# Kernel tuning notes

Hardware: AMD Instinct MI355X
Metric: run time of the kernel (lower is better)

Reference implementation:

```python
import jax, jax.numpy as jnp
import numpy as np

IMG = 14          # image_x_y_dim
STRIDE = 4        # stride == kernel_size == n_qubits
H_MAT = jnp.array([[1.0, 1.0], [1.0, -1.0]], dtype=jnp.complex64) / np.sqrt(2.0)
_RZ_SIGNS = jnp.array([-0.5j, 0.5j], dtype=jnp.complex64)


def _apply_1q(state, U, w):
    # contract 2x2 gate U into wire-axis w of state with shape (2,)*n
    s = jnp.tensordot(U, state, axes=[[1], [w]])
    return jnp.moveaxis(s, 0, w)


def _rz(state, theta, w, n):
    d = jnp.exp(_RZ_SIGNS * theta)  # diag(e^{-i t/2}, e^{i t/2})
    shape = [1] * n
    shape[w] = 2
    return state * d.reshape(shape)


def _rx(state, theta, w):
    c = jnp.cos(0.5 * theta).astype(jnp.complex64)
    s = ((-1j) * jnp.sin(0.5 * theta)).astype(jnp.complex64)
    U = jnp.stack([jnp.stack([c, s]), jnp.stack([s, c])])
    return _apply_1q(state, U, w)


def _ry(state, theta, w):
    c = jnp.cos(0.5 * theta).astype(jnp.complex64)
    s = jnp.sin(0.5 * theta).astype(jnp.complex64)
    U = jnp.stack([jnp.stack([c, -s]), jnp.stack([s, c])])
    return _apply_1q(state, U, w)


def _crz(state, theta, cw, tw, n):
    # PennyLane CRZ: diag(1, 1, e^{-i t/2}, e^{i t/2}) in |control, target> basis
    d = jnp.exp(_RZ_SIGNS * theta)
    P = jnp.stack([jnp.ones(2, jnp.complex64), d])  # axes: (control, target)
    if cw > tw:
        P = P.T
    a, b = min(cw, tw), max(cw, tw)
    shape = [1] * n
    shape[a] = 2
    shape[b] = 2
    return state * P.reshape(shape)


def _zexp(state, n):
    probs = state.real ** 2 + state.imag ** 2
    outs = []
    for w in range(n):
        shape = [1] * n
        shape[w] = 2
        sgn = jnp.array([1.0, -1.0], jnp.float32).reshape(shape)
        outs.append(jnp.sum(probs * sgn))
    return jnp.stack(outs)  # (n,)


def _circuit4(x, weights):
    # x: (L,) with L in {4, 8, 16}; weights: (2, 8)
    n, vpq, L = 4, 4, x.shape[0]
    state = jnp.zeros((2,) * n, jnp.complex64).at[(0,) * n].set(1.0)
    for q in range(n):  # encoding: H then alternating RZ/RX per qubit
        state = _apply_1q(state, H_MAT, q)
        for i in range(vpq):
            idx = q * vpq + i
            if idx < L:
                state = _rz(state, x[idx], q, n) if i % 2 == 0 else _rx(state, x[idx], q)
    for l in range(2):  # n_layers
        for i in range(n):
            state = _crz(state, weights[l, i], i, (i + 1) % n, n)
        for j in range(n, 2 * n):
            state = _ry(state, weights[l, j], j % n)
    return _zexp(state, n)  # (4,)


def _circuit8(x, weights):
    # x: (64,); weights: (3, 16); angles scaled by pi as in qnn_circuit
    n, L = 8, 64
    vpq = L // n + 1  # 9
    state = jnp.zeros((2,) * n, jnp.complex64).at[(0,) * n].set(1.0)
    for q in range(n):
        state = _apply_1q(state, H_MAT, q)
        for i in range(vpq):
            idx = q * vpq + i
            if idx < L:
                theta = np.pi * x[idx]
                state = _rz(state, theta, q, n) if i % 2 == 0 else _rx(state, theta, q)
    for l in range(3):  # qnn_layers
        for i in range(n):
            state = _crz(state, weights[l, i], i, (i + 1) % n, n)
        for j in range(n, 2 * n):
            state = _ry(state, weights[l, j], j % n)
    return _zexp(state, n)  # (8,)


def _forward_single(x196, w1, w2, fc_w, fc_b):
    img = x196.reshape(IMG, IMG)
    feats = []
    for i in range(0, IMG, STRIDE):
        for j in range(0, IMG, STRIDE):
            patch = img[i:i + 4, j:j + 4].reshape(-1)  # edge patches truncate to 8 or 4
            feats.append(_circuit4(patch, w1))
    f = jnp.concatenate(feats)       # (64,)
    g = _circuit8(f, w2)             # (8,)
    return fc_w @ g + fc_b           # (3,)


def setup_inputs() -> dict:
    key = jax.random.key(0)
    k0, k1, k2, k3, k4 = jax.random.split(key, 5)
    bs = 8192
    X = jax.random.normal(k0, (bs, 196), jnp.float32)
    w1 = jax.random.uniform(k1, (2, 8), jnp.float32, 0.0, 2.0 * np.pi)
    w2 = jax.random.uniform(k2, (3, 16), jnp.float32, 0.0, 2.0 * np.pi)
    fc_w = jax.random.normal(k3, (3, 8), jnp.float32) / np.sqrt(8.0)
    fc_b = jax.random.normal(k4, (3,), jnp.float32) * 0.01
    return {"X": X, "w1": w1, "w2": w2, "fc_w": fc_w, "fc_b": fc_b}


def reference(X, w1, w2, fc_w, fc_b):
    return jax.vmap(_forward_single, in_axes=(0, None, None, None, None))(X, w1, w2, fc_w, fc_b)
```

## Files before the change

kernel.cpp:

```cpp
#include <hip/hip_runtime.h>

#define DEV __device__ __forceinline__

namespace {

typedef float f32x2 __attribute__((ext_vector_type(2)));

DEV f32x2 splat(float x){ f32x2 r; r.x = x; r.y = x; return r; }
DEV f32x2 csw(f32x2 a){ return __builtin_shufflevector(a, a, 1, 0); }
DEV f32x2 cmulv(f32x2 a, f32x2 b){
  f32x2 nt; nt.x = -b.y; nt.y = b.x;
  return splat(a.x)*b + splat(a.y)*nt;
}
DEV f32x2 cphase(f32x2 a, f32x2 cv, f32x2 sv){ return cv*a + sv*csw(a); }
DEV void halfsc(float th, float& c, float& s){ __sincosf(0.5f*th, &s, &c); }

constexpr float RSQRT2 = 0.70710678118654752440f;
constexpr float PI_F   = 3.14159265358979323846f;

template<int CTRL> DEV float qperm(float v){
  return __int_as_float(__builtin_amdgcn_mov_dpp(__float_as_int(v), CTRL, 0xF, 0xF, true));
}
template<int OFF> DEV float swzf(float v){
  return __int_as_float(__builtin_amdgcn_ds_swizzle(__float_as_int(v), OFF));
}
template<int B> DEV float shfx(float v){
  if constexpr (B==1)      return qperm<0xB1>(v);
  else if constexpr (B==2) return qperm<0x4E>(v);
  else if constexpr (B==4) return swzf<0x101F>(v);
  else if constexpr (B==8) return qperm<0x128>(v);
  else                     return swzf<0x401F>(v);
}

template<int NA> DEV void build_psi(f32x2 (&v)[2], const float* ang, float scale){
  v[0].x = RSQRT2; v[0].y = 0.f;
  v[1].x = RSQRT2; v[1].y = 0.f;
  #pragma unroll
  for (int i = 0; i < NA; ++i){
    float c, s; halfsc(scale * ang[i], c, s);
    f32x2 cv = splat(c);
    f32x2 sp; sp.x = s;  sp.y = -s;
    if ((i & 1) == 0){
      f32x2 sn; sn.x = -s; sn.y = s;
      v[0] = cv*v[0] + sp*csw(v[0]);
      v[1] = cv*v[1] + sn*csw(v[1]);
    } else {
      f32x2 t0 = csw(v[0]), t1 = csw(v[1]);
      v[0] = cv*v[0] + sp*t1;
      v[1] = cv*v[1] + sp*t0;
    }
  }
}

template<int S> DEV void ry_loc8(f32x2 (&a)[8], float2 cs){
  const float c = cs.x, s = cs.y;
  #pragma unroll
  for (int m = 0; m < 8; ++m) if (!(m & S)) {
    f32x2 u = a[m], v = a[m|S];
    a[m]   = splat(c)*u - splat(s)*v;
    a[m|S] = splat(s)*u + splat(c)*v;
  }
}
template<int MASK> DEV void ry_lane8(f32x2 (&a)[8], int r, float2 cs){
  const float c = cs.x;
  const float sg = (r & MASK) ? cs.y : -cs.y;
  #pragma unroll
  for (int m = 0; m < 8; ++m){
    f32x2 o; o.x = shfx<MASK>(a[m].x); o.y = shfx<MASK>(a[m].y);
    a[m] = splat(c)*a[m] + splat(sg)*o;
  }
}

DEV f32x2 tov(float2 v){ f32x2 r; r.x = v.x; r.y = v.y; return r; }

}

__global__ __launch_bounds__(256, 4)
void qnn_fused_kernel(const float* __restrict__ X,  const float* __restrict__ w1,
                      const float* __restrict__ w2, const float* __restrict__ fcw,
                      const float* __restrict__ fcb, float* __restrict__ out, int bs)
{
  __shared__ float4 Xlds4[8*49];
  __shared__ float  feats[8][80];
  __shared__ float4 p1chain[8][16][5];
  __shared__ float4 chain2[8][9];
  __shared__ float4 p1phi[2][2][8];
  __shared__ float2 p1ry[2][4];
  __shared__ float2 ryw[3][8];
  __shared__ float4 phi2[3*32*9];

  const int t  = threadIdx.x;
  const int sl = t >> 5;
  const int r  = t & 31;
  int sample = blockIdx.x * 8 + sl;
  if (sample >= bs) sample = bs - 1;

  {
    const float4* X4 = (const float4*)X;
    for (int idx = t; idx < 8*49; idx += 256){
      int s_ = idx / 49, e = idx - s_*49;
      int gs = blockIdx.x * 8 + s_;
      if (gs >= bs) gs = bs - 1;
      Xlds4[idx] = X4[(size_t)gs*49 + e];
    }
  }
  if (t < 32){
    const int l = t >> 4, Lb = (t >> 3) & 1, m = t & 7;
    const float h0 = 0.5f*w1[l*8+0], h1 = 0.5f*w1[l*8+1];
    const float h2 = 0.5f*w1[l*8+2], h3 = 0.5f*w1[l*8+3];
    const bool m4 = m & 4, m2 = m & 2, m1 = m & 1;
    float phi = 0.f;
    phi += Lb ? (m4 ? h0 : -h0) : 0.f;
    phi += m4 ? (m2 ? h1 : -h1) : 0.f;
    phi += m2 ? (m1 ? h2 : -h2) : 0.f;
    phi += m1 ? (Lb ? h3 : -h3) : 0.f;
    float c, s; __sincosf(phi, &s, &c);
    p1phi[l][Lb][m] = {c, c, -s, s};
  } else if (t < 40){
    const int j = t - 32, l = j >> 2, i = j & 3;
    float c, s; halfsc(w1[l*8 + 4 + i], c, s); p1ry[l][i] = {c, s};
  } else if (t < 64){
    const int j = t - 40, l = j >> 3, i = j & 7;
    float c, s; halfsc(w2[l*16 + 8 + i], c, s); ryw[l][i] = {c, s};
  }
  for (int idx = t; idx < 3*256; idx += 256){
    const int l = idx >> 8, rr = (idx >> 3) & 31, mm = idx & 7;
    const float* wl = w2 + l*16;
    const float h0 = 0.5f*wl[0], h1 = 0.5f*wl[1], h2 = 0.5f*wl[2], h3 = 0.5f*wl[3];
    const float h4 = 0.5f*wl[4], h5 = 0.5f*wl[5], h6 = 0.5f*wl[6], h7 = 0.5f*wl[7];
    const bool b16 = rr & 16, b8 = rr & 8, b4 = rr & 4, b2 = rr & 2, b1 = rr & 1;
    const bool m4 = mm & 4, m2 = mm & 2, m1 = mm & 1;
    float phi = 0.f;
    phi += b16 ? (b8 ? h0 : -h0) : 0.f;
    phi += b8  ? (b4 ? h1 : -h1) : 0.f;
    phi += b4  ? (b2 ? h2 : -h2) : 0.f;
    phi += b2  ? (b1 ? h3 : -h3) : 0.f;
    phi += b1  ? (m4 ? h4 : -h4) : 0.f;
    phi += m4  ? (m2 ? h5 : -h5) : 0.f;
    phi += m2  ? (m1 ? h6 : -h6) : 0.f;
    phi += m1  ? (b16 ? h7 : -h7) : 0.f;
    float c, s; __sincosf(phi, &s, &c);
    phi2[(l*32 + rr)*9 + mm] = {c, c, -s, s};
  }
  __syncthreads();

  #pragma unroll
  for (int jj = 0; jj < 2; ++jj){
    const int j = t + jj*256;
    const int s_ = j >> 6, p = (j >> 2) & 15, q = j & 3;
    const int pi = p >> 2, pj = p & 3;
    const int shift = (pj == 3) ? 1 : 2;
    const int cmask = (1 << shift) - 1;
    const int limit = ((pi == 3) ? 2 : 4) << shift;
    const float* Xf = (const float*)Xlds4 + s_*196;
    float ang[4];
    #pragma unroll
    for (int i = 0; i < 4; ++i){
      const int k = q*4 + i;
      int idx = (pi*4 + (k >> shift))*14 + pj*4 + (k & cmask);
      idx = idx > 195 ? 195 : idx;
      float v = Xf[idx];
      ang[i] = (k < limit) ? v : 0.f;
    }
    f32x2 v[2];
    build_psi<4>(v, ang, 1.0f);
    p1chain[s_][p][q] = {v[0].x, v[0].y, v[1].x, v[1].y};
  }
  __syncthreads();

  {
    const int p = r >> 1, Lb = r & 1;
    f32x2 ps[4][2];
    #pragma unroll
    for (int q = 0; q < 4; ++q){
      float4 f = p1chain[sl][p][q];
      ps[q][0].x = f.x; ps[q][0].y = f.y;
      ps[q][1].x = f.z; ps[q][1].y = f.w;
    }
    f32x2 a8[8];
    {
      f32x2 t12[4];
      #pragma unroll
      for (int j = 0; j < 4; ++j) t12[j] = cmulv(ps[1][j>>1], ps[2][j&1]);
      f32x2 base = Lb ? ps[0][1] : ps[0][0];
      f32x2 bt[4];
      #pragma unroll
      for (int j = 0; j < 4; ++j) bt[j] = cmulv(base, t12[j]);
      #pragma unroll
      for (int m = 0; m < 8; ++m) a8[m] = cmulv(bt[m>>1], ps[3][m&1]);
    }

    #pragma unroll
    for (int l = 0; l < 2; ++l){
      const float4* ph = &p1phi[l][Lb][0];
      #pragma unroll
      for (int m = 0; m < 8; ++m){
        float4 w = ph[m];
        f32x2 cv; cv.x = w.x; cv.y = w.y;
        f32x2 sv; sv.x = w.z; sv.y = w.w;
        a8[m] = cphase(a8[m], cv, sv);
      }
      ry_lane8<1>(a8, r, p1ry[l][0]);
      ry_loc8<4>(a8, p1ry[l][1]);
      ry_loc8<2>(a8, p1ry[l][2]);
      ry_loc8<1>(a8, p1ry[l][3]);
    }

    float pr8[8];
    #pragma unroll
    for (int m = 0; m < 8; ++m) pr8[m] = a8[m].x*a8[m].x + a8[m].y*a8[m].y;
    float s_loc = 0.f;
    #pragma unroll
    for (int m = 0; m < 8; ++m) s_loc += pr8[m];
    float e1 = 0.f, e2 = 0.f, e3 = 0.f;
    #pragma unroll
    for (int m = 0; m < 8; ++m){
      e1 += (m & 4) ? -pr8[m] : pr8[m];
      e2 += (m & 2) ? -pr8[m] : pr8[m];
      e3 += (m & 1) ? -pr8[m] : pr8[m];
    }
    float v0 = Lb ? -s_loc : s_loc;
    v0 += shfx<1>(v0); e1 += shfx<1>(e1); e2 += shfx<1>(e2); e3 += shfx<1>(e3);
    feats[sl][p*4 + 2*Lb + 0] = Lb ? e2 : v0;
    feats[sl][p*4 + 2*Lb + 1] = Lb ? e3 : e1;
    if (r < 16) feats[sl][64 + r] = 0.f;
  }
  __syncthreads();

  if (t < 64){
    const int s_ = t >> 3, c = t & 7;
    f32x2 v[2];
    build_psi<9>(v, &feats[s_][c*9], PI_F);
    chain2[s_][c] = {v[0].x, v[0].y, v[1].x, v[1].y};
  }
  __syncthreads();

  f32x2 a[8];
  {
    const float2* c2 = (const float2*)&chain2[sl][0];
    f32x2 e0 = tov(c2[0*2 + ((r>>4)&1)]);
    f32x2 e1 = tov(c2[1*2 + ((r>>3)&1)]);
    f32x2 e2 = tov(c2[2*2 + ((r>>2)&1)]);
    f32x2 e3 = tov(c2[3*2 + ((r>>1)&1)]);
    f32x2 e4 = tov(c2[4*2 + ( r    &1)]);
    f32x2 L  = cmulv(cmulv(cmulv(e0, e1), cmulv(e2, e3)), e4);

    float4 q5 = chain2[sl][5], q6 = chain2[sl][6], q7 = chain2[sl][7];
    f32x2 p5[2], p6[2], p7[2];
    p5[0].x=q5.x; p5[0].y=q5.y; p5[1].x=q5.z; p5[1].y=q5.w;
    p6[0].x=q6.x; p6[0].y=q6.y; p6[1].x=q6.z; p6[1].y=q6.w;
    p7[0].x=q7.x; p7[0].y=q7.y; p7[1].x=q7.z; p7[1].y=q7.w;
    f32x2 p56[4];
    #pragma unroll
    for (int j = 0; j < 4; ++j) p56[j] = cmulv(p5[j>>1], p6[j&1]);
    f32x2 Lp[4];
    #pragma unroll
    for (int j = 0; j < 4; ++j) Lp[j] = cmulv(L, p56[j]);
    #pragma unroll
    for (int m = 0; m < 8; ++m) a[m] = cmulv(Lp[m>>1], p7[m&1]);
  }

  #pragma unroll
  for (int l = 0; l < 3; ++l){
    const float4* ph = &phi2[(l*32 + r)*9];
    #pragma unroll
    for (int m = 0; m < 8; ++m){
      float4 w = ph[m];
      f32x2 cv; cv.x = w.x; cv.y = w.y;
      f32x2 sv; sv.x = w.z; sv.y = w.w;
      a[m] = cphase(a[m], cv, sv);
    }
    ry_lane8<16>(a, r, ryw[l][0]);
    ry_lane8<8>(a, r, ryw[l][1]);
    ry_lane8<4>(a, r, ryw[l][2]);
    ry_lane8<2>(a, r, ryw[l][3]);
    ry_lane8<1>(a, r, ryw[l][4]);
    ry_loc8<4>(a, ryw[l][5]);
    ry_loc8<2>(a, ryw[l][6]);
    ry_loc8<1>(a, ryw[l][7]);
  }

  float pr8[8];
  #pragma unroll
  for (int m = 0; m < 8; ++m) pr8[m] = a[m].x*a[m].x + a[m].y*a[m].y;
  float s_loc = 0.f;
  #pragma unroll
  for (int m = 0; m < 8; ++m) s_loc += pr8[m];
  float e5 = 0.f, e6 = 0.f, e7 = 0.f;
  #pragma unroll
  for (int m = 0; m < 8; ++m){
    e5 += (m & 4) ? -pr8[m] : pr8[m];
    e6 += (m & 2) ? -pr8[m] : pr8[m];
    e7 += (m & 1) ? -pr8[m] : pr8[m];
  }
  float gp[8];
  gp[0] = (r & 16) ? -s_loc : s_loc;
  gp[1] = (r &  8) ? -s_loc : s_loc;
  gp[2] = (r &  4) ? -s_loc : s_loc;
  gp[3] = (r &  2) ? -s_loc : s_loc;
  gp[4] = (r &  1) ? -s_loc : s_loc;
  gp[5] = e5; gp[6] = e6; gp[7] = e7;

  float o0 = 0.f, o1 = 0.f, o2 = 0.f;
  #pragma unroll
  for (int w = 0; w < 8; ++w){
    o0 += fcw[0*8 + w] * gp[w];
    o1 += fcw[1*8 + w] * gp[w];
    o2 += fcw[2*8 + w] * gp[w];
  }
  o0 += shfx<1>(o0);  o1 += shfx<1>(o1);  o2 += shfx<1>(o2);
  o0 += shfx<2>(o0);  o1 += shfx<2>(o1);  o2 += shfx<2>(o2);
  o0 += shfx<4>(o0);  o1 += shfx<4>(o1);  o2 += shfx<4>(o2);
  o0 += shfx<8>(o0);  o1 += shfx<8>(o1);  o2 += shfx<8>(o2);
  o0 += shfx<16>(o0); o1 += shfx<16>(o1); o2 += shfx<16>(o2);

  if (r < 3){
    float o = (r == 0) ? o0 : ((r == 1) ? o1 : o2);
    out[(size_t)sample*3 + r] = o + fcb[r];
  }
}

extern "C" void kernel_launch(void* const* d_in, const int* in_sizes, int n_in,
                              void* d_out, int out_size, void* d_ws, size_t ws_size,
                              hipStream_t stream)
{
  const float* X   = (const float*)d_in[0];
  const float* w1  = (const float*)d_in[1];
  const float* w2  = (const float*)d_in[2];
  const float* fcw = (const float*)d_in[3];
  const float* fcb = (const float*)d_in[4];
  float* out = (float*)d_out;
  const int bs = in_sizes[0] / 196;
  const int blocks = (bs + 7) / 8;
  hipLaunchKernelGGL(qnn_fused_kernel, dim3(blocks), dim3(256), 0, stream,
                     X, w1, w2, fcw, fcb, out, bs);
}
```

Baseline: 18.19 us.

## Process two samples per 32-lane group to amortize gate setup and ILP

Each 32-lane group now simulates two samples at once, so a block handles 16 samples instead of 8 and the grid is halved. Gate coefficients, phase tables and RY parameters are loaded once and applied to both state vectors, and the two independent state updates interleave for more instruction-level parallelism. In exchange it doubles register state per thread, lowers the launch bound occupancy hint from 4 to 2 waves, and increases LDS per block, which may reduce latency hiding.

Result: slower. 18.99 us (+4.4%).

```diff
diff --git a/kernel.cpp b/kernel.cpp
--- a/kernel.cpp
+++ b/kernel.cpp
@@ -52,22 +52,28 @@
   }
 }
 
-template<int S> DEV void ry_loc8(f32x2 (&a)[8], float2 cs){
+template<int S> DEV void ry_loc8_2(f32x2 (&a)[2][8], float2 cs){
   const float c = cs.x, s = cs.y;
   #pragma unroll
   for (int m = 0; m < 8; ++m) if (!(m & S)) {
-    f32x2 u = a[m], v = a[m|S];
-    a[m]   = splat(c)*u - splat(s)*v;
-    a[m|S] = splat(s)*u + splat(c)*v;
-  }
-}
-template<int MASK> DEV void ry_lane8(f32x2 (&a)[8], int r, float2 cs){
+    #pragma unroll
+    for (int st = 0; st < 2; ++st){
+      f32x2 u = a[st][m], v = a[st][m|S];
+      a[st][m]   = splat(c)*u - splat(s)*v;
+      a[st][m|S] = splat(s)*u + splat(c)*v;
+    }
+  }
+}
+template<int MASK> DEV void ry_lane8_2(f32x2 (&a)[2][8], int r, float2 cs){
   const float c = cs.x;
   const float sg = (r & MASK) ? cs.y : -cs.y;
   #pragma unroll
   for (int m = 0; m < 8; ++m){
-    f32x2 o; o.x = shfx<MASK>(a[m].x); o.y = shfx<MASK>(a[m].y);
-    a[m] = splat(c)*a[m] + splat(sg)*o;
+    #pragma unroll
+    for (int st = 0; st < 2; ++st){
+      f32x2 o; o.x = shfx<MASK>(a[st][m].x); o.y = shfx<MASK>(a[st][m].y);
+      a[st][m] = splat(c)*a[st][m] + splat(sg)*o;
+    }
   }
 }
 
@@ -75,31 +81,33 @@
 
 }
 
-__global__ __launch_bounds__(256, 4)
+__global__ __launch_bounds__(256, 2)
 void qnn_fused_kernel(const float* __restrict__ X,  const float* __restrict__ w1,
                       const float* __restrict__ w2, const float* __restrict__ fcw,
                       const float* __restrict__ fcb, float* __restrict__ out, int bs)
 {
-  __shared__ float4 Xlds4[8*49];
-  __shared__ float  feats[8][80];
-  __shared__ float4 p1chain[8][16][5];
-  __shared__ float4 chain2[8][9];
+  __shared__ float4 Xlds4[16*49];
+  __shared__ float  feats[16][80];
+  __shared__ float4 p1chain[16][16][5];
+  __shared__ float4 chain2[16][9];
   __shared__ float4 p1phi[2][2][8];
   __shared__ float2 p1ry[2][4];
   __shared__ float2 ryw[3][8];
   __shared__ float4 phi2[3*32*9];
 
   const int t  = threadIdx.x;
-  const int sl = t >> 5;
+  const int g  = t >> 5;
   const int r  = t & 31;
-  int sample = blockIdx.x * 8 + sl;
-  if (sample >= bs) sample = bs - 1;
+  int sA = blockIdx.x * 16 + 2*g;
+  int sB = sA + 1;
+  if (sA >= bs) sA = bs - 1;
+  if (sB >= bs) sB = bs - 1;
 
   {
     const float4* X4 = (const float4*)X;
-    for (int idx = t; idx < 8*49; idx += 256){
+    for (int idx = t; idx < 16*49; idx += 256){
       int s_ = idx / 49, e = idx - s_*49;
-      int gs = blockIdx.x * 8 + s_;
+      int gs = blockIdx.x * 16 + s_;
       if (gs >= bs) gs = bs - 1;
       Xlds4[idx] = X4[(size_t)gs*49 + e];
     }
@@ -145,7 +153,7 @@
   __syncthreads();
 
   #pragma unroll
-  for (int jj = 0; jj < 2; ++jj){
+  for (int jj = 0; jj < 4; ++jj){
     const int j = t + jj*256;
     const int s_ = j >> 6, p = (j >> 2) & 15, q = j & 3;
     const int pi = p >> 2, pj = p & 3;
@@ -170,15 +178,16 @@
 
   {
     const int p = r >> 1, Lb = r & 1;
-    f32x2 ps[4][2];
-    #pragma unroll
-    for (int q = 0; q < 4; ++q){
-      float4 f = p1chain[sl][p][q];
-      ps[q][0].x = f.x; ps[q][0].y = f.y;
-      ps[q][1].x = f.z; ps[q][1].y = f.w;
-    }
-    f32x2 a8[8];
-    {
+    f32x2 a8[2][8];
+    #pragma unroll
+    for (int st = 0; st < 2; ++st){
+      f32x2 ps[4][2];
+      #pragma unroll
+      for (int q = 0; q < 4; ++q){
+        float4 fq = p1chain[2*g + st][p][q];
+        ps[q][0].x = fq.x; ps[q][0].y = fq.y;
+        ps[q][1].x = fq.z; ps[q][1].y = fq.w;
+      }
       f32x2 t12[4];
       #pragma unroll
       for (int j = 0; j < 4; ++j) t12[j] = cmulv(ps[1][j>>1], ps[2][j&1]);
@@ -187,7 +196,7 @@
       #pragma unroll
       for (int j = 0; j < 4; ++j) bt[j] = cmulv(base, t12[j]);
       #pragma unroll
-      for (int m = 0; m < 8; ++m) a8[m] = cmulv(bt[m>>1], ps[3][m&1]);
+      for (int m = 0; m < 8; ++m) a8[st][m] = cmulv(bt[m>>1], ps[3][m&1]);
     }
 
     #pragma unroll
@@ -198,36 +207,40 @@
         float4 w = ph[m];
         f32x2 cv; cv.x = w.x; cv.y = w.y;
         f32x2 sv; sv.x = w.z; sv.y = w.w;
-        a8[m] = cphase(a8[m], cv, sv);
+        a8[0][m] = cphase(a8[0][m], cv, sv);
+        a8[1][m] = cphase(a8[1][m], cv, sv);
       }
-      ry_lane8<1>(a8, r, p1ry[l][0]);
-      ry_loc8<4>(a8, p1ry[l][1]);
-      ry_loc8<2>(a8, p1ry[l][2]);
-      ry_loc8<1>(a8, p1ry[l][3]);
-    }
-
-    float pr8[8];
-    #pragma unroll
-    for (int m = 0; m < 8; ++m) pr8[m] = a8[m].x*a8[m].x + a8[m].y*a8[m].y;
-    float s_loc = 0.f;
-    #pragma unroll
-    for (int m = 0; m < 8; ++m) s_loc += pr8[m];
-    float e1 = 0.f, e2 = 0.f, e3 = 0.f;
-    #pragma unroll
-    for (int m = 0; m < 8; ++m){
-      e1 += (m & 4) ? -pr8[m] : pr8[m];
-      e2 += (m & 2) ? -pr8[m] : pr8[m];
-      e3 += (m & 1) ? -pr8[m] : pr8[m];
-    }
-    float v0 = Lb ? -s_loc : s_loc;
-    v0 += shfx<1>(v0); e1 += shfx<1>(e1); e2 += shfx<1>(e2); e3 += shfx<1>(e3);
-    feats[sl][p*4 + 2*Lb + 0] = Lb ? e2 : v0;
-    feats[sl][p*4 + 2*Lb + 1] = Lb ? e3 : e1;
-    if (r < 16) feats[sl][64 + r] = 0.f;
+      ry_lane8_2<1>(a8, r, p1ry[l][0]);
+      ry_loc8_2<4>(a8, p1ry[l][1]);
+      ry_loc8_2<2>(a8, p1ry[l][2]);
+      ry_loc8_2<1>(a8, p1ry[l][3]);
+    }
+
+    #pragma unroll
+    for (int st = 0; st < 2; ++st){
+      float pr8[8];
+      #pragma unroll
+      for (int m = 0; m < 8; ++m) pr8[m] = a8[st][m].x*a8[st][m].x + a8[st][m].y*a8[st][m].y;
+      float s_loc = 0.f;
+      #pragma unroll
+      for (int m = 0; m < 8; ++m) s_loc += pr8[m];
+      float e1 = 0.f, e2 = 0.f, e3 = 0.f;
+      #pragma unroll
+      for (int m = 0; m < 8; ++m){
+        e1 += (m & 4) ? -pr8[m] : pr8[m];
+        e2 += (m & 2) ? -pr8[m] : pr8[m];
+        e3 += (m & 1) ? -pr8[m] : pr8[m];
+      }
+      float v0 = Lb ? -s_loc : s_loc;
+      v0 += shfx<1>(v0); e1 += shfx<1>(e1); e2 += shfx<1>(e2); e3 += shfx<1>(e3);
+      feats[2*g + st][p*4 + 2*Lb + 0] = Lb ? e2 : v0;
+      feats[2*g + st][p*4 + 2*Lb + 1] = Lb ? e3 : e1;
+    }
+    if (r < 16){ feats[2*g][64 + r] = 0.f; feats[2*g + 1][64 + r] = 0.f; }
   }
   __syncthreads();
 
-  if (t < 64){
+  if (t < 128){
     const int s_ = t >> 3, c = t & 7;
     f32x2 v[2];
     build_psi<9>(v, &feats[s_][c*9], PI_F);
@@ -235,9 +248,10 @@
   }
   __syncthreads();
 
-  f32x2 a[8];
-  {
-    const float2* c2 = (const float2*)&chain2[sl][0];
+  f32x2 a[2][8];
+  #pragma unroll
+  for (int st = 0; st < 2; ++st){
+    const float2* c2 = (const float2*)&chain2[2*g + st][0];
     f32x2 e0 = tov(c2[0*2 + ((r>>4)&1)]);
     f32x2 e1 = tov(c2[1*2 + ((r>>3)&1)]);
     f32x2 e2 = tov(c2[2*2 + ((r>>2)&1)]);
@@ -245,7 +259,7 @@
     f32x2 e4 = tov(c2[4*2 + ( r    &1)]);
     f32x2 L  = cmulv(cmulv(cmulv(e0, e1), cmulv(e2, e3)), e4);
 
-    float4 q5 = chain2[sl][5], q6 = chain2[sl][6], q7 = chain2[sl][7];
+    float4 q5 = chain2[2*g + st][5], q6 = chain2[2*g + st][6], q7 = chain2[2*g + st][7];
     f32x2 p5[2], p6[2], p7[2];
     p5[0].x=q5.x; p5[0].y=q5.y; p5[1].x=q5.z; p5[1].y=q5.w;
     p6[0].x=q6.x; p6[0].y=q6.y; p6[1].x=q6.z; p6[1].y=q6.w;
@@ -257,7 +271,7 @@
     #pragma unroll
     for (int j = 0; j < 4; ++j) Lp[j] = cmulv(L, p56[j]);
     #pragma unroll
-    for (int m = 0; m < 8; ++m) a[m] = cmulv(Lp[m>>1], p7[m&1]);
+    for (int m = 0; m < 8; ++m) a[st][m] = cmulv(Lp[m>>1], p7[m&1]);
   }
 
   #pragma unroll
@@ -268,55 +282,67 @@
       float4 w = ph[m];
       f32x2 cv; cv.x = w.x; cv.y = w.y;
       f32x2 sv; sv.x = w.z; sv.y = w.w;
-      a[m] = cphase(a[m], cv, sv);
-    }
-    ry_lane8<16>(a, r, ryw[l][0]);
-    ry_lane8<8>(a, r, ryw[l][1]);
-    ry_lane8<4>(a, r, ryw[l][2]);
-    ry_lane8<2>(a, r, ryw[l][3]);
-    ry_lane8<1>(a, r, ryw[l][4]);
-    ry_loc8<4>(a, ryw[l][5]);
-    ry_loc8<2>(a, ryw[l][6]);
-    ry_loc8<1>(a, ryw[l][7]);
-  }
-
-  float pr8[8];
-  #pragma unroll
-  for (int m = 0; m < 8; ++m) pr8[m] = a[m].x*a[m].x + a[m].y*a[m].y;
-  float s_loc = 0.f;
-  #pragma unroll
-  for (int m = 0; m < 8; ++m) s_loc += pr8[m];
-  float e5 = 0.f, e6 = 0.f, e7 = 0.f;
-  #pragma unroll
-  for (int m = 0; m < 8; ++m){
-    e5 += (m & 4) ? -pr8[m] : pr8[m];
-    e6 += (m & 2) ? -pr8[m] : pr8[m];
-    e7 += (m & 1) ? -pr8[m] : pr8[m];
-  }
-  float gp[8];
-  gp[0] = (r & 16) ? -s_loc : s_loc;
-  gp[1] = (r &  8) ? -s_loc : s_loc;
-  gp[2] = (r &  4) ? -s_loc : s_loc;
-  gp[3] = (r &  2) ? -s_loc : s_loc;
-  gp[4] = (r &  1) ? -s_loc : s_loc;
-  gp[5] = e5; gp[6] = e6; gp[7] = e7;
-
-  float o0 = 0.f, o1 = 0.f, o2 = 0.f;
-  #pragma unroll
-  for (int w = 0; w < 8; ++w){
-    o0 += fcw[0*8 + w] * gp[w];
-    o1 += fcw[1*8 + w] * gp[w];
-    o2 += fcw[2*8 + w] * gp[w];
-  }
-  o0 += shfx<1>(o0);  o1 += shfx<1>(o1);  o2 += shfx<1>(o2);
-  o0 += shfx<2>(o0);  o1 += shfx<2>(o1);  o2 += shfx<2>(o2);
-  o0 += shfx<4>(o0);  o1 += shfx<4>(o1);  o2 += shfx<4>(o2);
-  o0 += shfx<8>(o0);  o1 += shfx<8>(o1);  o2 += shfx<8>(o2);
-  o0 += shfx<16>(o0); o1 += shfx<16>(o1); o2 += shfx<16>(o2);
-
+      a[0][m] = cphase(a[0][m], cv, sv);
+      a[1][m] = cphase(a[1][m], cv, sv);
+    }
+    ry_lane8_2<16>(a, r, ryw[l][0]);
+    ry_lane8_2<8>(a, r, ryw[l][1]);
+    ry_lane8_2<4>(a, r, ryw[l][2]);
+    ry_lane8_2<2>(a, r, ryw[l][3]);
+    ry_lane8_2<1>(a, r, ryw[l][4]);
+    ry_loc8_2<4>(a, ryw[l][5]);
+    ry_loc8_2<2>(a, ryw[l][6]);
+    ry_loc8_2<1>(a, ryw[l][7]);
+  }
+
+  float oo[2][3];
+  #pragma unroll
+  for (int st = 0; st < 2; ++st){
+    float pr8[8];
+    #pragma unroll
+    for (int m = 0; m < 8; ++m) pr8[m] = a[st][m].x*a[st][m].x + a[st][m].y*a[st][m].y;
+    float s_loc = 0.f;
+    #pragma unroll
+    for (int m = 0; m < 8; ++m) s_loc += pr8[m];
+    float e5 = 0.f, e6 = 0.f, e7 = 0.f;
+    #pragma unroll
+    for (int m = 0; m < 8; ++m){
+      e5 += (m & 4) ? -pr8[m] : pr8[m];
+      e6 += (m & 2) ? -pr8[m] : pr8[m];
+      e7 += (m & 1) ? -pr8[m] : pr8[m];
+    }
+    float gp[8];
+    gp[0] = (r & 16) ? -s_loc : s_loc;
+    gp[1] = (r &  8) ? -s_loc : s_loc;
+    gp[2] = (r &  4) ? -s_loc : s_loc;
+    gp[3] = (r &  2) ? -s_loc : s_loc;
+    gp[4] = (r &  1) ? -s_loc : s_loc;
+    gp[5] = e5; gp[6] = e6; gp[7] = e7;
+
+    float o0 = 0.f, o1 = 0.f, o2 = 0.f;
+    #pragma unroll
+    for (int w = 0; w < 8; ++w){
+      o0 += fcw[0*8 + w] * gp[w];
+      o1 += fcw[1*8 + w] * gp[w];
+      o2 += fcw[2*8 + w] * gp[w];
+    }
+    oo[st][0] = o0; oo[st][1] = o1; oo[st][2] = o2;
+  }
+  #pragma unroll
+  for (int k = 0; k < 3; ++k){
+    float vA = oo[0][k], vB = oo[1][k];
+    vA += shfx<1>(vA);  vB += shfx<1>(vB);
+    vA += shfx<2>(vA);  vB += shfx<2>(vB);
+    vA += shfx<4>(vA);  vB += shfx<4>(vB);
+    vA += shfx<8>(vA);  vB += shfx<8>(vB);
+    vA += shfx<16>(vA); vB += shfx<16>(vB);
+    oo[0][k] = vA; oo[1][k] = vB;
+  }
   if (r < 3){
-    float o = (r == 0) ? o0 : ((r == 1) ? o1 : o2);
-    out[(size_t)sample*3 + r] = o + fcb[r];
+    out[(size_t)sA*3 + r] = oo[0][r] + fcb[r];
+  } else if (r >= 4 && r < 7){
+    const int k = r - 4;
+    out[(size_t)sB*3 + k] = oo[1][k] + fcb[k];
   }
 }
 
@@ -331,7 +357,7 @@
   const float* fcb = (const float*)d_in[4];
   float* out = (float*)d_out;
   const int bs = in_sizes[0] / 196;
-  const int blocks = (bs + 7) / 8;
+  const int blocks = (bs + 15) / 16;
   hipLaunchKernelGGL(qnn_fused_kernel, dim3(blocks), dim3(256), 0, stream,
                      X, w1, w2, fcw, fcb, out, bs);
 }
```

## Split statevectors across 64 lanes per sample with 4-amplitude registers

Applied to the files above, without the earlier changes.

Each sample now uses a full 64-lane wavefront instead of 32 lanes, so each lane holds 4 amplitudes instead of 8. The first-stage circuits use 4 lanes per patch. The CRZ phase tables shrink to float2 entries applied with a complex multiply. The LDS staging of X is dropped in favour of direct global reads, and the launch bound is raised to 8 blocks per SM with 4 samples per block. The aim is to cut per-thread registers and serial work to raise occupancy, at the cost of more cross-lane shuffles (including a shfl_xor by 32), twice as many blocks, and uncoalesced direct X loads.

Measured after the change: 21.53 us. 18.3% more time.

```diff
diff --git a/kernel.cpp b/kernel.cpp
--- a/kernel.cpp
+++ b/kernel.cpp
@@ -12,7 +12,6 @@
   f32x2 nt; nt.x = -b.y; nt.y = b.x;
   return splat(a.x)*b + splat(a.y)*nt;
 }
-DEV f32x2 cphase(f32x2 a, f32x2 cv, f32x2 sv){ return cv*a + sv*csw(a); }
 DEV void halfsc(float th, float& c, float& s){ __sincosf(0.5f*th, &s, &c); }
 
 constexpr float RSQRT2 = 0.70710678118654752440f;
@@ -25,11 +24,12 @@
   return __int_as_float(__builtin_amdgcn_ds_swizzle(__float_as_int(v), OFF));
 }
 template<int B> DEV float shfx(float v){
-  if constexpr (B==1)      return qperm<0xB1>(v);
-  else if constexpr (B==2) return qperm<0x4E>(v);
-  else if constexpr (B==4) return swzf<0x101F>(v);
-  else if constexpr (B==8) return qperm<0x128>(v);
-  else                     return swzf<0x401F>(v);
+  if constexpr (B==1)       return qperm<0xB1>(v);
+  else if constexpr (B==2)  return qperm<0x4E>(v);
+  else if constexpr (B==4)  return swzf<0x101F>(v);
+  else if constexpr (B==8)  return qperm<0x128>(v);
+  else if constexpr (B==16) return swzf<0x401F>(v);
+  else                      return __shfl_xor(v, 32);
 }
 
 template<int NA> DEV void build_psi(f32x2 (&v)[2], const float* ang, float scale){
@@ -52,20 +52,20 @@
   }
 }
 
-template<int S> DEV void ry_loc8(f32x2 (&a)[8], float2 cs){
+template<int S> DEV void ry_loc4(f32x2 (&a)[4], float2 cs){
   const float c = cs.x, s = cs.y;
   #pragma unroll
-  for (int m = 0; m < 8; ++m) if (!(m & S)) {
+  for (int m = 0; m < 4; ++m) if (!(m & S)) {
     f32x2 u = a[m], v = a[m|S];
     a[m]   = splat(c)*u - splat(s)*v;
     a[m|S] = splat(s)*u + splat(c)*v;
   }
 }
-template<int MASK> DEV void ry_lane8(f32x2 (&a)[8], int r, float2 cs){
+template<int MASK> DEV void ry_lane4(f32x2 (&a)[4], int r, float2 cs){
   const float c = cs.x;
   const float sg = (r & MASK) ? cs.y : -cs.y;
   #pragma unroll
-  for (int m = 0; m < 8; ++m){
+  for (int m = 0; m < 4; ++m){
     f32x2 o; o.x = shfx<MASK>(a[m].x); o.y = shfx<MASK>(a[m].y);
     a[m] = splat(c)*a[m] + splat(sg)*o;
   }
@@ -75,84 +75,72 @@
 
 }
 
-__global__ __launch_bounds__(256, 4)
+__global__ __launch_bounds__(256, 8)
 void qnn_fused_kernel(const float* __restrict__ X,  const float* __restrict__ w1,
                       const float* __restrict__ w2, const float* __restrict__ fcw,
                       const float* __restrict__ fcb, float* __restrict__ out, int bs)
 {
-  __shared__ float4 Xlds4[8*49];
-  __shared__ float  feats[8][80];
-  __shared__ float4 p1chain[8][16][5];
-  __shared__ float4 chain2[8][9];
-  __shared__ float4 p1phi[2][2][8];
+  __shared__ float2 phi2[3*64*5];
+  __shared__ float2 p1phi[2][4][4];
   __shared__ float2 p1ry[2][4];
   __shared__ float2 ryw[3][8];
-  __shared__ float4 phi2[3*32*9];
+  __shared__ float4 p1chain[4][16][5];
+  __shared__ float4 chain2[4][9];
+  __shared__ float  feats[4][80];
 
   const int t  = threadIdx.x;
-  const int sl = t >> 5;
-  const int r  = t & 31;
-  int sample = blockIdx.x * 8 + sl;
+  const int sl = t >> 6;
+  const int r  = t & 63;
+  int sample = blockIdx.x * 4 + sl;
   if (sample >= bs) sample = bs - 1;
 
-  {
-    const float4* X4 = (const float4*)X;
-    for (int idx = t; idx < 8*49; idx += 256){
-      int s_ = idx / 49, e = idx - s_*49;
-      int gs = blockIdx.x * 8 + s_;
-      if (gs >= bs) gs = bs - 1;
-      Xlds4[idx] = X4[(size_t)gs*49 + e];
-    }
+  #pragma unroll
+  for (int j = 0; j < 3; ++j){
+    const int idx = t + j*256;
+    const int l = idx >> 8, rr = (idx >> 2) & 63, mm = idx & 3;
+    const float* wl = w2 + l*16;
+    float h[8];
+    #pragma unroll
+    for (int i = 0; i < 8; ++i) h[i] = 0.5f*wl[i];
+    bool b[8];
+    b[0]=(rr>>5)&1; b[1]=(rr>>4)&1; b[2]=(rr>>3)&1;
+    b[3]=(rr>>2)&1; b[4]=(rr>>1)&1; b[5]=rr&1;
+    b[6]=(mm>>1)&1; b[7]=mm&1;
+    float phi = 0.f;
+    #pragma unroll
+    for (int i = 0; i < 8; ++i)
+      phi += b[i] ? (b[(i+1)&7] ? h[i] : -h[i]) : 0.f;
+    float c, s; __sincosf(phi, &s, &c);
+    phi2[(l*64 + rr)*5 + mm] = {c, s};
   }
   if (t < 32){
-    const int l = t >> 4, Lb = (t >> 3) & 1, m = t & 7;
+    const int l = t >> 4, ll = (t >> 2) & 3, mm = t & 3;
     const float h0 = 0.5f*w1[l*8+0], h1 = 0.5f*w1[l*8+1];
     const float h2 = 0.5f*w1[l*8+2], h3 = 0.5f*w1[l*8+3];
-    const bool m4 = m & 4, m2 = m & 2, m1 = m & 1;
+    const bool b0 = ll & 2, b1 = ll & 1, b2 = mm & 2, b3 = mm & 1;
     float phi = 0.f;
-    phi += Lb ? (m4 ? h0 : -h0) : 0.f;
-    phi += m4 ? (m2 ? h1 : -h1) : 0.f;
-    phi += m2 ? (m1 ? h2 : -h2) : 0.f;
-    phi += m1 ? (Lb ? h3 : -h3) : 0.f;
+    phi += b0 ? (b1 ? h0 : -h0) : 0.f;
+    phi += b1 ? (b2 ? h1 : -h1) : 0.f;
+    phi += b2 ? (b3 ? h2 : -h2) : 0.f;
+    phi += b3 ? (b0 ? h3 : -h3) : 0.f;
     float c, s; __sincosf(phi, &s, &c);
-    p1phi[l][Lb][m] = {c, c, -s, s};
-  } else if (t < 40){
-    const int j = t - 32, l = j >> 2, i = j & 3;
+    p1phi[l][ll][mm] = {c, s};
+  } else if (t < 56){
+    const int j = t - 32, l = j >> 3, i = j & 7;
+    float c, s; halfsc(w2[l*16 + 8 + i], c, s); ryw[l][i] = {c, s};
+  } else if (t < 64){
+    const int j = t - 56, l = j >> 2, i = j & 3;
     float c, s; halfsc(w1[l*8 + 4 + i], c, s); p1ry[l][i] = {c, s};
-  } else if (t < 64){
-    const int j = t - 40, l = j >> 3, i = j & 7;
-    float c, s; halfsc(w2[l*16 + 8 + i], c, s); ryw[l][i] = {c, s};
-  }
-  for (int idx = t; idx < 3*256; idx += 256){
-    const int l = idx >> 8, rr = (idx >> 3) & 31, mm = idx & 7;
-    const float* wl = w2 + l*16;
-    const float h0 = 0.5f*wl[0], h1 = 0.5f*wl[1], h2 = 0.5f*wl[2], h3 = 0.5f*wl[3];
-    const float h4 = 0.5f*wl[4], h5 = 0.5f*wl[5], h6 = 0.5f*wl[6], h7 = 0.5f*wl[7];
-    const bool b16 = rr & 16, b8 = rr & 8, b4 = rr & 4, b2 = rr & 2, b1 = rr & 1;
-    const bool m4 = mm & 4, m2 = mm & 2, m1 = mm & 1;
-    float phi = 0.f;
-    phi += b16 ? (b8 ? h0 : -h0) : 0.f;
-    phi += b8  ? (b4 ? h1 : -h1) : 0.f;
-    phi += b4  ? (b2 ? h2 : -h2) : 0.f;
-    phi += b2  ? (b1 ? h3 : -h3) : 0.f;
-    phi += b1  ? (m4 ? h4 : -h4) : 0.f;
-    phi += m4  ? (m2 ? h5 : -h5) : 0.f;
-    phi += m2  ? (m1 ? h6 : -h6) : 0.f;
-    phi += m1  ? (b16 ? h7 : -h7) : 0.f;
-    float c, s; __sincosf(phi, &s, &c);
-    phi2[(l*32 + rr)*9 + mm] = {c, c, -s, s};
-  }
-  __syncthreads();
-
-  #pragma unroll
-  for (int jj = 0; jj < 2; ++jj){
-    const int j = t + jj*256;
-    const int s_ = j >> 6, p = (j >> 2) & 15, q = j & 3;
+  }
+  __syncthreads();
+
+  {
+    const int p = r >> 2, q = r & 3;
     const int pi = p >> 2, pj = p & 3;
     const int shift = (pj == 3) ? 1 : 2;
     const int cmask = (1 << shift) - 1;
     const int limit = ((pi == 3) ? 2 : 4) << shift;
-    const float* Xf = (const float*)Xlds4 + s_*196;
+    const float* Xf = X + (size_t)sample * 196;
     float ang[4];
     #pragma unroll
     for (int i = 0; i < 4; ++i){
@@ -164,70 +152,53 @@
     }
     f32x2 v[2];
     build_psi<4>(v, ang, 1.0f);
-    p1chain[s_][p][q] = {v[0].x, v[0].y, v[1].x, v[1].y};
+    p1chain[sl][p][q] = {v[0].x, v[0].y, v[1].x, v[1].y};
   }
   __syncthreads();
 
   {
-    const int p = r >> 1, Lb = r & 1;
+    const int p = r >> 2, ll = r & 3;
     f32x2 ps[4][2];
     #pragma unroll
     for (int q = 0; q < 4; ++q){
-      float4 f = p1chain[sl][p][q];
-      ps[q][0].x = f.x; ps[q][0].y = f.y;
-      ps[q][1].x = f.z; ps[q][1].y = f.w;
-    }
-    f32x2 a8[8];
-    {
-      f32x2 t12[4];
+      float4 fq = p1chain[sl][p][q];
+      ps[q][0].x = fq.x; ps[q][0].y = fq.y;
+      ps[q][1].x = fq.z; ps[q][1].y = fq.w;
+    }
+    f32x2 L = cmulv(ps[0][(ll>>1)&1], ps[1][ll&1]);
+    f32x2 a4[4];
+    #pragma unroll
+    for (int m = 0; m < 4; ++m) a4[m] = cmulv(L, cmulv(ps[2][m>>1], ps[3][m&1]));
+
+    #pragma unroll
+    for (int l = 0; l < 2; ++l){
       #pragma unroll
-      for (int j = 0; j < 4; ++j) t12[j] = cmulv(ps[1][j>>1], ps[2][j&1]);
-      f32x2 base = Lb ? ps[0][1] : ps[0][0];
-      f32x2 bt[4];
-      #pragma unroll
-      for (int j = 0; j < 4; ++j) bt[j] = cmulv(base, t12[j]);
-      #pragma unroll
-      for (int m = 0; m < 8; ++m) a8[m] = cmulv(bt[m>>1], ps[3][m&1]);
-    }
-
-    #pragma unroll
-    for (int l = 0; l < 2; ++l){
-      const float4* ph = &p1phi[l][Lb][0];
-      #pragma unroll
-      for (int m = 0; m < 8; ++m){
-        float4 w = ph[m];
-        f32x2 cv; cv.x = w.x; cv.y = w.y;
-        f32x2 sv; sv.x = w.z; sv.y = w.w;
-        a8[m] = cphase(a8[m], cv, sv);
-      }
-      ry_lane8<1>(a8, r, p1ry[l][0]);
-      ry_loc8<4>(a8, p1ry[l][1]);
-      ry_loc8<2>(a8, p1ry[l][2]);
-      ry_loc8<1>(a8, p1ry[l][3]);
-    }
-
-    float pr8[8];
-    #pragma unroll
-    for (int m = 0; m < 8; ++m) pr8[m] = a8[m].x*a8[m].x + a8[m].y*a8[m].y;
-    float s_loc = 0.f;
-    #pragma unroll
-    for (int m = 0; m < 8; ++m) s_loc += pr8[m];
-    float e1 = 0.f, e2 = 0.f, e3 = 0.f;
-    #pragma unroll
-    for (int m = 0; m < 8; ++m){
-      e1 += (m & 4) ? -pr8[m] : pr8[m];
-      e2 += (m & 2) ? -pr8[m] : pr8[m];
-      e3 += (m & 1) ? -pr8[m] : pr8[m];
-    }
-    float v0 = Lb ? -s_loc : s_loc;
-    v0 += shfx<1>(v0); e1 += shfx<1>(e1); e2 += shfx<1>(e2); e3 += shfx<1>(e3);
-    feats[sl][p*4 + 2*Lb + 0] = Lb ? e2 : v0;
-    feats[sl][p*4 + 2*Lb + 1] = Lb ? e3 : e1;
+      for (int m = 0; m < 4; ++m) a4[m] = cmulv(a4[m], tov(p1phi[l][ll][m]));
+      ry_lane4<2>(a4, r, p1ry[l][0]);
+      ry_lane4<1>(a4, r, p1ry[l][1]);
+      ry_loc4<2>(a4, p1ry[l][2]);
+      ry_loc4<1>(a4, p1ry[l][3]);
+    }
+
+    float pr4[4];
+    #pragma unroll
+    for (int m = 0; m < 4; ++m) pr4[m] = a4[m].x*a4[m].x + a4[m].y*a4[m].y;
+    const float s_loc = pr4[0] + pr4[1] + pr4[2] + pr4[3];
+    float z0 = (ll & 2) ? -s_loc : s_loc;
+    float z1 = (ll & 1) ? -s_loc : s_loc;
+    float z2 = pr4[0] + pr4[1] - pr4[2] - pr4[3];
+    float z3 = pr4[0] - pr4[1] + pr4[2] - pr4[3];
+    z0 += shfx<1>(z0); z0 += shfx<2>(z0);
+    z1 += shfx<1>(z1); z1 += shfx<2>(z1);
+    z2 += shfx<1>(z2); z2 += shfx<2>(z2);
+    z3 += shfx<1>(z3); z3 += shfx<2>(z3);
+    float zv = (ll == 0) ? z0 : (ll == 1) ? z1 : (ll == 2) ? z2 : z3;
+    feats[sl][p*4 + ll] = zv;
     if (r < 16) feats[sl][64 + r] = 0.f;
   }
   __syncthreads();
 
-  if (t < 64){
+  if (t < 32){
     const int s_ = t >> 3, c = t & 7;
     f32x2 v[2];
     build_psi<9>(v, &feats[s_][c*9], PI_F);
@@ -235,71 +206,53 @@
   }
   __syncthreads();
 
-  f32x2 a[8];
+  f32x2 a[4];
   {
     const float2* c2 = (const float2*)&chain2[sl][0];
-    f32x2 e0 = tov(c2[0*2 + ((r>>4)&1)]);
-    f32x2 e1 = tov(c2[1*2 + ((r>>3)&1)]);
-    f32x2 e2 = tov(c2[2*2 + ((r>>2)&1)]);
-    f32x2 e3 = tov(c2[3*2 + ((r>>1)&1)]);
-    f32x2 e4 = tov(c2[4*2 + ( r    &1)]);
-    f32x2 L  = cmulv(cmulv(cmulv(e0, e1), cmulv(e2, e3)), e4);
-
-    float4 q5 = chain2[sl][5], q6 = chain2[sl][6], q7 = chain2[sl][7];
-    f32x2 p5[2], p6[2], p7[2];
-    p5[0].x=q5.x; p5[0].y=q5.y; p5[1].x=q5.z; p5[1].y=q5.w;
+    f32x2 e0 = tov(c2[0*2 + ((r>>5)&1)]);
+    f32x2 e1 = tov(c2[1*2 + ((r>>4)&1)]);
+    f32x2 e2 = tov(c2[2*2 + ((r>>3)&1)]);
+    f32x2 e3 = tov(c2[3*2 + ((r>>2)&1)]);
+    f32x2 e4 = tov(c2[4*2 + ((r>>1)&1)]);
+    f32x2 e5 = tov(c2[5*2 + ( r    &1)]);
+    f32x2 L  = cmulv(cmulv(cmulv(e0, e1), cmulv(e2, e3)), cmulv(e4, e5));
+
+    float4 q6 = chain2[sl][6], q7 = chain2[sl][7];
+    f32x2 p6[2], p7[2];
     p6[0].x=q6.x; p6[0].y=q6.y; p6[1].x=q6.z; p6[1].y=q6.w;
     p7[0].x=q7.x; p7[0].y=q7.y; p7[1].x=q7.z; p7[1].y=q7.w;
-    f32x2 p56[4];
-    #pragma unroll
-    for (int j = 0; j < 4; ++j) p56[j] = cmulv(p5[j>>1], p6[j&1]);
-    f32x2 Lp[4];
-    #pragma unroll
-    for (int j = 0; j < 4; ++j) Lp[j] = cmulv(L, p56[j]);
-    #pragma unroll
-    for (int m = 0; m < 8; ++m) a[m] = cmulv(Lp[m>>1], p7[m&1]);
+    #pragma unroll
+    for (int m = 0; m < 4; ++m) a[m] = cmulv(L, cmulv(p6[m>>1], p7[m&1]));
   }
 
   #pragma unroll
   for (int l = 0; l < 3; ++l){
-    const float4* ph = &phi2[(l*32 + r)*9];
-    #pragma unroll
-    for (int m = 0; m < 8; ++m){
-      float4 w = ph[m];
-      f32x2 cv; cv.x = w.x; cv.y = w.y;
-      f32x2 sv; sv.x = w.z; sv.y = w.w;
-      a[m] = cphase(a[m], cv, sv);
-    }
-    ry_lane8<16>(a, r, ryw[l][0]);
-    ry_lane8<8>(a, r, ryw[l][1]);
-    ry_lane8<4>(a, r, ryw[l][2]);
-    ry_lane8<2>(a, r, ryw[l][3]);
-    ry_lane8<1>(a, r, ryw[l][4]);
-    ry_loc8<4>(a, ryw[l][5]);
-    ry_loc8<2>(a, ryw[l][6]);
-    ry_loc8<1>(a, ryw[l][7]);
-  }
-
-  float pr8[8];
-  #pragma unroll
-  for (int m = 0; m < 8; ++m) pr8[m] = a[m].x*a[m].x + a[m].y*a[m].y;
-  float s_loc = 0.f;
-  #pragma unroll
-  for (int m = 0; m < 8; ++m) s_loc += pr8[m];
-  float e5 = 0.f, e6 = 0.f, e7 = 0.f;
-  #pragma unroll
-  for (int m = 0; m < 8; ++m){
-    e5 += (m & 4) ? -pr8[m] : pr8[m];
-    e6 += (m & 2) ? -pr8[m] : pr8[m];
-    e7 += (m & 1) ? -pr8[m] : pr8[m];
-  }
+    const float2* ph = &phi2[(l*64 + r)*5];
+    #pragma unroll
+    for (int m = 0; m < 4; ++m) a[m] = cmulv(a[m], tov(ph[m]));
+    ry_lane4<32>(a, r, ryw[l][0]);
+    ry_lane4<16>(a, r, ryw[l][1]);
+    ry_lane4<8>(a, r, ryw[l][2]);
+    ry_lane4<4>(a, r, ryw[l][3]);
+    ry_lane4<2>(a, r, ryw[l][4]);
+    ry_lane4<1>(a, r, ryw[l][5]);
+    ry_loc4<2>(a, ryw[l][6]);
+    ry_loc4<1>(a, ryw[l][7]);
+  }
+
+  float pr4[4];
+  #pragma unroll
+  for (int m = 0; m < 4; ++m) pr4[m] = a[m].x*a[m].x + a[m].y*a[m].y;
+  const float s_loc = pr4[0] + pr4[1] + pr4[2] + pr4[3];
   float gp[8];
-  gp[0] = (r & 16) ? -s_loc : s_loc;
-  gp[1] = (r &  8) ? -s_loc : s_loc;
-  gp[2] = (r &  4) ? -s_loc : s_loc;
-  gp[3] = (r &  2) ? -s_loc : s_loc;
-  gp[4] = (r &  1) ? -s_loc : s_loc;
-  gp[5] = e5; gp[6] = e6; gp[7] = e7;
+  gp[0] = (r & 32) ? -s_loc : s_loc;
+  gp[1] = (r & 16) ? -s_loc : s_loc;
+  gp[2] = (r &  8) ? -s_loc : s_loc;
+  gp[3] = (r &  4) ? -s_loc : s_loc;
+  gp[4] = (r &  2) ? -s_loc : s_loc;
+  gp[5] = (r &  1) ? -s_loc : s_loc;
+  gp[6] = pr4[0] + pr4[1] - pr4[2] - pr4[3];
+  gp[7] = pr4[0] - pr4[1] + pr4[2] - pr4[3];
 
   float o0 = 0.f, o1 = 0.f, o2 = 0.f;
   #pragma unroll
@@ -313,6 +266,7 @@
   o0 += shfx<4>(o0);  o1 += shfx<4>(o1);  o2 += shfx<4>(o2);
   o0 += shfx<8>(o0);  o1 += shfx<8>(o1);  o2 += shfx<8>(o2);
   o0 += shfx<16>(o0); o1 += shfx<16>(o1); o2 += shfx<16>(o2);
+  o0 += shfx<32>(o0); o1 += shfx<32>(o1); o2 += shfx<32>(o2);
 
   if (r < 3){
     float o = (r == 0) ? o0 : ((r == 1) ? o1 : o2);
@@ -331,7 +285,7 @@
   const float* fcb = (const float*)d_in[4];
   float* out = (float*)d_out;
   const int bs = in_sizes[0] / 196;
-  const int blocks = (bs + 7) / 8;
+  const int blocks = (bs + 3) / 4;
   hipLaunchKernelGGL(qnn_fused_kernel, dim3(blocks), dim3(256), 0, stream,
                      X, w1, w2, fcw, fcb, out, bs);
 }
```

## Split 9-gate chain build across two thread groups and read X directly from global

Applied to the files above, without the earlier changes.

Splits the serial 9-gate single-qubit chain that builds each stage-2 qubit state into two halves run by separate threads. The second half is applied as an SU(2) matrix and composed with the first half's state, adding a sync and a small combine step. It also drops the LDS staging of X, together with one barrier, in favour of direct global loads in the patch stage. Launch bounds are raised to 5 blocks per SM to allow more occupancy, which risks register pressure and uncoalesced global reads.

After: 17.99 us. Within noise of the previous version (-1.1%).

```diff
diff --git a/kernel.cpp b/kernel.cpp
--- a/kernel.cpp
+++ b/kernel.cpp
@@ -12,6 +12,7 @@
   f32x2 nt; nt.x = -b.y; nt.y = b.x;
   return splat(a.x)*b + splat(a.y)*nt;
 }
+DEV f32x2 cconj(f32x2 a){ a.y = -a.y; return a; }
 DEV f32x2 cphase(f32x2 a, f32x2 cv, f32x2 sv){ return cv*a + sv*csw(a); }
 DEV void halfsc(float th, float& c, float& s){ __sincosf(0.5f*th, &s, &c); }
 
@@ -32,12 +33,10 @@
   else                     return swzf<0x401F>(v);
 }
 
-template<int NA> DEV void build_psi(f32x2 (&v)[2], const float* ang, float scale){
-  v[0].x = RSQRT2; v[0].y = 0.f;
-  v[1].x = RSQRT2; v[1].y = 0.f;
-  #pragma unroll
-  for (int i = 0; i < NA; ++i){
-    float c, s; halfsc(scale * ang[i], c, s);
+template<int I0, int N> DEV void run_gates(f32x2 (&v)[2], const float* f, float scale){
+  #pragma unroll
+  for (int i = I0; i < I0 + N; ++i){
+    float c, s; halfsc(scale * f[i], c, s);
     f32x2 cv = splat(c);
     f32x2 sp; sp.x = s;  sp.y = -s;
     if ((i & 1) == 0){
@@ -51,6 +50,11 @@
     }
   }
 }
+template<int N> DEV void build_psi(f32x2 (&v)[2], const float* ang, float scale){
+  v[0].x = RSQRT2; v[0].y = 0.f;
+  v[1].x = RSQRT2; v[1].y = 0.f;
+  run_gates<0, N>(v, ang, scale);
+}
 
 template<int S> DEV void ry_loc8(f32x2 (&a)[8], float2 cs){
   const float c = cs.x, s = cs.y;
@@ -75,14 +79,14 @@
 
 }
 
-__global__ __launch_bounds__(256, 4)
+__global__ __launch_bounds__(256, 5)
 void qnn_fused_kernel(const float* __restrict__ X,  const float* __restrict__ w1,
                       const float* __restrict__ w2, const float* __restrict__ fcw,
                       const float* __restrict__ fcb, float* __restrict__ out, int bs)
 {
-  __shared__ float4 Xlds4[8*49];
   __shared__ float  feats[8][80];
   __shared__ float4 p1chain[8][16][5];
+  __shared__ float4 chainH[8][8][2];
   __shared__ float4 chain2[8][9];
   __shared__ float4 p1phi[2][2][8];
   __shared__ float2 p1ry[2][4];
@@ -95,15 +99,6 @@
   int sample = blockIdx.x * 8 + sl;
   if (sample >= bs) sample = bs - 1;
 
-  {
-    const float4* X4 = (const float4*)X;
-    for (int idx = t; idx < 8*49; idx += 256){
-      int s_ = idx / 49, e = idx - s_*49;
-      int gs = blockIdx.x * 8 + s_;
-      if (gs >= bs) gs = bs - 1;
-      Xlds4[idx] = X4[(size_t)gs*49 + e];
-    }
-  }
   if (t < 32){
     const int l = t >> 4, Lb = (t >> 3) & 1, m = t & 7;
     const float h0 = 0.5f*w1[l*8+0], h1 = 0.5f*w1[l*8+1];
@@ -142,7 +137,6 @@
     float c, s; __sincosf(phi, &s, &c);
     phi2[(l*32 + rr)*9 + mm] = {c, c, -s, s};
   }
-  __syncthreads();
 
   #pragma unroll
   for (int jj = 0; jj < 2; ++jj){
@@ -152,7 +146,9 @@
     const int shift = (pj == 3) ? 1 : 2;
     const int cmask = (1 << shift) - 1;
     const int limit = ((pi == 3) ? 2 : 4) << shift;
-    const float* Xf = (const float*)Xlds4 + s_*196;
+    int gs = blockIdx.x * 8 + s_;
+    if (gs >= bs) gs = bs - 1;
+    const float* Xf = X + (size_t)gs * 196;
     float ang[4];
     #pragma unroll
     for (int i = 0; i < 4; ++i){
@@ -173,9 +169,9 @@
     f32x2 ps[4][2];
     #pragma unroll
     for (int q = 0; q < 4; ++q){
-      float4 f = p1chain[sl][p][q];
-      ps[q][0].x = f.x; ps[q][0].y = f.y;
-      ps[q][1].x = f.z; ps[q][1].y = f.w;
+      float4 fq = p1chain[sl][p][q];
+      ps[q][0].x = fq.x; ps[q][0].y = fq.y;
+      ps[q][1].x = fq.z; ps[q][1].y = fq.w;
     }
     f32x2 a8[8];
     {
@@ -227,11 +223,30 @@
   }
   __syncthreads();
 
+  if (t < 128){
+    const int h = t >> 6, jj = t & 63;
+    const int s_ = jj >> 3, c = jj & 7;
+    const float* f = &feats[s_][c*9];
+    f32x2 v[2];
+    if (h == 0){
+      build_psi<5>(v, f, PI_F);
+    } else {
+      v[0].x = 1.f; v[0].y = 0.f;
+      v[1].x = 0.f; v[1].y = 0.f;
+      run_gates<5, 4>(v, f, PI_F);
+    }
+    chainH[s_][c][h] = {v[0].x, v[0].y, v[1].x, v[1].y};
+  }
+  __syncthreads();
   if (t < 64){
     const int s_ = t >> 3, c = t & 7;
-    f32x2 v[2];
-    build_psi<9>(v, &feats[s_][c*9], PI_F);
-    chain2[s_][c] = {v[0].x, v[0].y, v[1].x, v[1].y};
+    float4 A = chainH[s_][c][0], B = chainH[s_][c][1];
+    f32x2 vA0, vA1, al, be;
+    vA0.x=A.x; vA0.y=A.y; vA1.x=A.z; vA1.y=A.w;
+    al.x=B.x;  al.y=B.y;  be.x=B.z;  be.y=B.w;
+    f32x2 v0 = cmulv(al, vA0) - cmulv(cconj(be), vA1);
+    f32x2 v1 = cmulv(be, vA0) + cmulv(cconj(al), vA1);
+    chain2[s_][c] = {v0.x, v0.y, v1.x, v1.y};
   }
   __syncthreads();
 
```
